# Performance work log

Measured on AMD Instinct MI355X. Metric: run time of the kernel, lower is better.

Reference implementation:

```python
import jax, jax.numpy as jnp
import numpy as np

LN_EPS = 1e-5
K = 6
NUM_KP = 5


def decoder_res_cat(x, w1, b1, gamma, beta, w2, b2):
    # MLP = relu(LayerNorm(Linear(x))); out = Linear(cat([x, MLP(x)]))
    h = x @ w1 + b1
    mu = h.mean(axis=-1, keepdims=True)
    var = ((h - mu) ** 2).mean(axis=-1, keepdims=True)
    h = jax.nn.relu(gamma * (h - mu) / jnp.sqrt(var + LN_EPS) + beta)
    return jnp.concatenate([x, h], axis=-1) @ w2 + b2


def setup_inputs() -> dict:
    key = jax.random.key(0)
    ks = jax.random.split(key, 8)
    B, S, E, H = 2048, 134, 256, 1024
    s = 0.02
    return {
        "hidden_output": jax.random.normal(ks[0], (B, S, E), jnp.float32),
        "future_key_points": jax.random.normal(ks[1], (B, NUM_KP, 2), jnp.float32),
        "ld_w1": jax.random.normal(ks[2], (E, H), jnp.float32) * s,
        "ld_b1": jnp.zeros((H,), jnp.float32),
        "ld_gamma": jnp.ones((H,), jnp.float32),
        "ld_beta": jnp.zeros((H,), jnp.float32),
        "ld_w2": jax.random.normal(ks[3], (E + H, 2 * K), jnp.float32) * s,
        "ld_b2": jnp.zeros((2 * K,), jnp.float32),
        "sd_w1": jax.random.normal(ks[4], (E, H), jnp.float32) * s,
        "sd_b1": jnp.zeros((H,), jnp.float32),
        "sd_gamma": jnp.ones((H,), jnp.float32),
        "sd_beta": jnp.zeros((H,), jnp.float32),
        "sd_w2": jax.random.normal(ks[5], (E + H, K), jnp.float32) * s,
        "sd_b2": jnp.zeros((K,), jnp.float32),
        "context_length": 128,
    }


def reference(hidden_output, future_key_points, ld_w1, ld_b1, ld_gamma, ld_beta,
              ld_w2, ld_b2, sd_w1, sd_b1, sd_gamma, sd_beta, sd_w2, sd_b2,
              context_length):
    B, T = future_key_points.shape[0], future_key_points.shape[1]
    kp_start = context_length - 1  # use_proposal=False
    h = jax.lax.dynamic_slice_in_dim(hidden_output, kp_start, T, axis=1)  # [B,T,E]

    logits = decoder_res_cat(h, ld_w1, ld_b1, ld_gamma, ld_beta, ld_w2, ld_b2)
    logits = logits.reshape(B, T, K, 2)                                   # [B,T,K,2]
    scores = decoder_res_cat(h, sd_w1, sd_b1, sd_gamma, sd_beta, sd_w2, sd_b2)  # [B,T,K]

    # per-mode MSE(reduction='none') summed over xy -> [B,T,K]
    sq = (logits - future_key_points[:, :, None, :2]) ** 2
    loss_bk = sq.sum(axis=-1)
    min_loss = loss_bk.min(axis=-1)           # [B,T]
    min_idx = loss_bk.argmin(axis=-1)         # [B,T] int

    # CrossEntropyLoss applied to softmax(scores) (faithful double-softmax)
    sm = jax.nn.softmax(scores, axis=-1)
    logp = jax.nn.log_softmax(sm, axis=-1)
    ce = -jnp.take_along_axis(logp, min_idx[..., None], axis=-1)[..., 0]  # [B,T]

    weights = 0.1 ** (4.0 - jnp.arange(T, dtype=jnp.float32))             # [T]
    loss_per_kp = min_loss.mean(axis=0) * weights + ce.mean(axis=0)       # [T]

    selected = jnp.take_along_axis(logits, min_idx[:, :, None, None], axis=2)[:, :, 0, :]  # [B,T,2]
    kp_loss = loss_per_kp.mean() * 1.0  # kp_loss_rescale=1.0
    return kp_loss, logits, scores, selected, loss_per_kp
```

## Files before the change

### kernel.cpp

```cpp
#include <hip/hip_runtime.h>
#include <math.h>

#define B_    2048
#define S_    134
#define E_    256
#define H_    1024
#define T_    5
#define KK_   6
#define NROWS (B_*T_)
#define R_    8
#define NBLK  (NROWS/R_)

#define OFF_LOGITS 1
#define OFF_SCORES (OFF_LOGITS + NROWS*12)
#define OFF_SEL    (OFF_SCORES + NROWS*6)
#define OFF_LPK    (OFF_SEL + NROWS*2)

template<int NOUT>
__device__ __forceinline__ void decoder_phase(
    const float (*xs)[E_],
    const float* __restrict__ w1, const float* __restrict__ b1,
    const float* __restrict__ ga, const float* __restrict__ be,
    const float* __restrict__ w2, const float* __restrict__ b2,
    float (*hs)[H_], float (*red)[4][2], float* mu_s, float* rs_s,
    float* osh, float* __restrict__ gout, int g0, int tid)
{
    const int wave = tid >> 6;
    const int lane = tid & 63;
    const int j0   = tid * 4;

    float acc[R_][4];
#pragma unroll
    for (int r = 0; r < R_; ++r) {
        acc[r][0] = 0.f; acc[r][1] = 0.f; acc[r][2] = 0.f; acc[r][3] = 0.f;
    }

    for (int k0 = 0; k0 < E_; k0 += 8) {
        float4 w[8];
#pragma unroll
        for (int kk = 0; kk < 8; ++kk)
            w[kk] = *(const float4*)(w1 + (size_t)(k0 + kk)*H_ + j0);
#pragma unroll
        for (int r = 0; r < R_; ++r) {
            float4 xa = *(const float4*)&xs[r][k0];
            float4 xb = *(const float4*)&xs[r][k0+4];
            acc[r][0] += xa.x*w[0].x; acc[r][1] += xa.x*w[0].y; acc[r][2] += xa.x*w[0].z; acc[r][3] += xa.x*w[0].w;
            acc[r][0] += xa.y*w[1].x; acc[r][1] += xa.y*w[1].y; acc[r][2] += xa.y*w[1].z; acc[r][3] += xa.y*w[1].w;
            acc[r][0] += xa.z*w[2].x; acc[r][1] += xa.z*w[2].y; acc[r][2] += xa.z*w[2].z; acc[r][3] += xa.z*w[2].w;
            acc[r][0] += xa.w*w[3].x; acc[r][1] += xa.w*w[3].y; acc[r][2] += xa.w*w[3].z; acc[r][3] += xa.w*w[3].w;
            acc[r][0] += xb.x*w[4].x; acc[r][1] += xb.x*w[4].y; acc[r][2] += xb.x*w[4].z; acc[r][3] += xb.x*w[4].w;
            acc[r][0] += xb.y*w[5].x; acc[r][1] += xb.y*w[5].y; acc[r][2] += xb.y*w[5].z; acc[r][3] += xb.y*w[5].w;
            acc[r][0] += xb.z*w[6].x; acc[r][1] += xb.z*w[6].y; acc[r][2] += xb.z*w[6].z; acc[r][3] += xb.z*w[6].w;
            acc[r][0] += xb.w*w[7].x; acc[r][1] += xb.w*w[7].y; acc[r][2] += xb.w*w[7].z; acc[r][3] += xb.w*w[7].w;
        }
    }

    {
        float4 bv = *(const float4*)(b1 + j0);
#pragma unroll
        for (int r = 0; r < R_; ++r) {
            acc[r][0] += bv.x; acc[r][1] += bv.y; acc[r][2] += bv.z; acc[r][3] += bv.w;
        }
    }

#pragma unroll
    for (int r = 0; r < R_; ++r) {
        float s  = acc[r][0] + acc[r][1] + acc[r][2] + acc[r][3];
        float ss = acc[r][0]*acc[r][0] + acc[r][1]*acc[r][1]
                 + acc[r][2]*acc[r][2] + acc[r][3]*acc[r][3];
#pragma unroll
        for (int off = 32; off > 0; off >>= 1) {
            s  += __shfl_xor(s,  off, 64);
            ss += __shfl_xor(ss, off, 64);
        }
        if (lane == 0) { red[r][wave][0] = s; red[r][wave][1] = ss; }
    }
    __syncthreads();
    if (tid < R_) {
        float s  = red[tid][0][0] + red[tid][1][0] + red[tid][2][0] + red[tid][3][0];
        float ss = red[tid][0][1] + red[tid][1][1] + red[tid][2][1] + red[tid][3][1];
        float mu  = s * (1.0f / H_);
        float var = ss * (1.0f / H_) - mu * mu;
        mu_s[tid] = mu;
        rs_s[tid] = rsqrtf(var + 1e-5f);
    }
    __syncthreads();

    {
        float4 gv = *(const float4*)(ga + j0);
        float4 bv = *(const float4*)(be + j0);
#pragma unroll
        for (int r = 0; r < R_; ++r) {
            float mu = mu_s[r], rs = rs_s[r];
            float4 hv;
            hv.x = gv.x * ((acc[r][0] - mu) * rs) + bv.x;
            hv.y = gv.y * ((acc[r][1] - mu) * rs) + bv.y;
            hv.z = gv.z * ((acc[r][2] - mu) * rs) + bv.z;
            hv.w = gv.w * ((acc[r][3] - mu) * rs) + bv.w;
            hv.x = hv.x > 0.f ? hv.x : 0.f;
            hv.y = hv.y > 0.f ? hv.y : 0.f;
            hv.z = hv.z > 0.f ? hv.z : 0.f;
            hv.w = hv.w > 0.f ? hv.w : 0.f;
            *(float4*)&hs[r][j0] = hv;
        }
    }
    __syncthreads();

    float p[2][NOUT];
#pragma unroll
    for (int rr = 0; rr < 2; ++rr)
#pragma unroll
        for (int n = 0; n < NOUT; ++n) p[rr][n] = 0.f;

    const int jbase = lane * 20;
#pragma unroll
    for (int jj = 0; jj < 20; ++jj) {
        const int j = jbase + jj;
        float w2r[NOUT];
#pragma unroll
        for (int n = 0; n < NOUT; ++n) w2r[n] = w2[(size_t)j*NOUT + n];
#pragma unroll
        for (int rr = 0; rr < 2; ++rr) {
            const int r = wave*2 + rr;
            float v = (j < E_) ? xs[r][j] : hs[r][j - E_];
#pragma unroll
            for (int n = 0; n < NOUT; ++n) p[rr][n] += v * w2r[n];
        }
    }
#pragma unroll
    for (int rr = 0; rr < 2; ++rr)
#pragma unroll
        for (int n = 0; n < NOUT; ++n)
#pragma unroll
            for (int off = 32; off > 0; off >>= 1)
                p[rr][n] += __shfl_xor(p[rr][n], off, 64);

    if (lane == 0) {
#pragma unroll
        for (int rr = 0; rr < 2; ++rr) {
            const int r = wave*2 + rr;
            const int g = g0 + r;
#pragma unroll
            for (int n = 0; n < NOUT; ++n) {
                float v = p[rr][n] + b2[n];
                osh[r*NOUT + n] = v;
                gout[(size_t)g*NOUT + n] = v;
            }
        }
    }
    __syncthreads();
}

__global__ __launch_bounds__(256, 3)
void kp_fused(const float* __restrict__ hid,  const float* __restrict__ fkp,
              const float* __restrict__ w1ld, const float* __restrict__ b1ld,
              const float* __restrict__ gld,  const float* __restrict__ btld,
              const float* __restrict__ w2ld, const float* __restrict__ b2ld,
              const float* __restrict__ w1sd, const float* __restrict__ b1sd,
              const float* __restrict__ gsd,  const float* __restrict__ btsd,
              const float* __restrict__ w2sd, const float* __restrict__ b2sd,
              const int* __restrict__ ctx,
              float* __restrict__ out, float* __restrict__ ws)
{
    __shared__ float hs[R_][H_];
    __shared__ float xs[R_][E_];
    __shared__ float red[R_][4][2];
    __shared__ float mu_s[R_], rs_s[R_];
    __shared__ float lo_s[R_*12];
    __shared__ float sc_s[R_*6];

    const int tid = threadIdx.x;
    const int g0  = blockIdx.x * R_;
    const int kp0 = ctx[0] - 1;

    {
        const int r   = tid >> 5;
        const int off = (tid & 31) * 8;
        const int g = g0 + r;
        const int b = g / T_;
        const int t = g - b * T_;
        const float* src = hid + (size_t)(b * S_ + kp0 + t) * E_ + off;
        float4 v0 = *(const float4*)(src);
        float4 v1 = *(const float4*)(src + 4);
        *(float4*)&xs[r][off]     = v0;
        *(float4*)&xs[r][off + 4] = v1;
    }
    __syncthreads();

    decoder_phase<12>(xs, w1ld, b1ld, gld, btld, w2ld, b2ld,
                      hs, red, mu_s, rs_s, lo_s, out + OFF_LOGITS, g0, tid);
    decoder_phase<6>(xs, w1sd, b1sd, gsd, btsd, w2sd, b2sd,
                     hs, red, mu_s, rs_s, sc_s, out + OFF_SCORES, g0, tid);

    if (tid < R_) {
        const int g = g0 + tid;
        const int b = g / T_;
        const int t = g - b * T_;
        const float y0 = fkp[b*(T_*2) + t*2 + 0];
        const float y1 = fkp[b*(T_*2) + t*2 + 1];

        float best = 1e30f; int am = 0;
#pragma unroll
        for (int k = 0; k < KK_; ++k) {
            float dx = lo_s[tid*12 + 2*k + 0] - y0;
            float dy = lo_s[tid*12 + 2*k + 1] - y1;
            float L = dx*dx + dy*dy;
            if (L < best) { best = L; am = k; }
        }

        float m = -1e30f;
#pragma unroll
        for (int k = 0; k < KK_; ++k) m = fmaxf(m, sc_s[tid*6 + k]);
        float e[KK_]; float ssum = 0.f;
#pragma unroll
        for (int k = 0; k < KK_; ++k) { e[k] = expf(sc_s[tid*6 + k] - m); ssum += e[k]; }
        const float inv = 1.0f / ssum;
        float lse = 0.f, sm_am = 0.f;
#pragma unroll
        for (int k = 0; k < KK_; ++k) {
            float smk = e[k] * inv;
            lse += expf(smk);
            if (k == am) sm_am = smk;
        }
        const float ce = logf(lse) - sm_am;

        out[OFF_SEL + g*2 + 0] = lo_s[tid*12 + 2*am + 0];
        out[OFF_SEL + g*2 + 1] = lo_s[tid*12 + 2*am + 1];

        atomicAdd(&ws[t],       best);
        atomicAdd(&ws[T_ + t],  ce);
    }
}

__global__ void kp_finalize(const float* __restrict__ ws, float* __restrict__ out)
{
    if (threadIdx.x == 0 && blockIdx.x == 0) {
        const float wts[T_] = {1e-4f, 1e-3f, 1e-2f, 1e-1f, 1.0f};
        float s = 0.f;
#pragma unroll
        for (int t = 0; t < T_; ++t) {
            float ml = ws[t]      * (1.0f / B_);
            float ce = ws[T_ + t] * (1.0f / B_);
            float l  = ml * wts[t] + ce;
            out[OFF_LPK + t] = l;
            s += l;
        }
        out[0] = s * (1.0f / T_);
    }
}

extern "C" void kernel_launch(void* const* d_in, const int* in_sizes, int n_in,
                              void* d_out, int out_size, void* d_ws, size_t ws_size,
                              hipStream_t stream)
{
    const float* hid  = (const float*)d_in[0];
    const float* fkp  = (const float*)d_in[1];
    const float* w1ld = (const float*)d_in[2];
    const float* b1ld = (const float*)d_in[3];
    const float* gld  = (const float*)d_in[4];
    const float* btld = (const float*)d_in[5];
    const float* w2ld = (const float*)d_in[6];
    const float* b2ld = (const float*)d_in[7];
    const float* w1sd = (const float*)d_in[8];
    const float* b1sd = (const float*)d_in[9];
    const float* gsd  = (const float*)d_in[10];
    const float* btsd = (const float*)d_in[11];
    const float* w2sd = (const float*)d_in[12];
    const float* b2sd = (const float*)d_in[13];
    const int*   ctx  = (const int*)d_in[14];
    float* out = (float*)d_out;
    float* ws  = (float*)d_ws;

    hipMemsetAsync(ws, 0, 2 * T_ * sizeof(float), stream);

    kp_fused<<<NBLK, 256, 0, stream>>>(hid, fkp,
                                       w1ld, b1ld, gld, btld, w2ld, b2ld,
                                       w1sd, b1sd, gsd, btsd, w2sd, b2sd,
                                       ctx, out, ws);
    kp_finalize<<<1, 64, 0, stream>>>(ws, out);
}
```

Before: 536.0 us.

## Halve hidden LDS buffer with two-pass second GEMM, double-buffer W1 loads

The hidden activation buffer in shared memory shrinks from 1024 to 512 columns per row. The second linear layer now runs in two passes: the first half of the hidden columns (plus x) is consumed, then the second half is written into the same buffer and consumed. W1 loads in the first GEMM are double-buffered with a software-pipelined prefetch, and launch bounds are raised to 4 blocks per CU. This is meant to cut LDS per block and hide global-load latency so occupancy rises. In exchange it adds extra barriers and may increase register pressure from the second W1 buffer under the tighter occupancy target.

```diff
diff --git a/kernel.cpp b/kernel.cpp
--- a/kernel.cpp
+++ b/kernel.cpp
@@ -5,6 +5,7 @@
 #define S_    134
 #define E_    256
 #define H_    1024
+#define HH_   512
 #define T_    5
 #define KK_   6
 #define NROWS (B_*T_)
@@ -22,7 +23,7 @@
     const float* __restrict__ w1, const float* __restrict__ b1,
     const float* __restrict__ ga, const float* __restrict__ be,
     const float* __restrict__ w2, const float* __restrict__ b2,
-    float (*hs)[H_], float (*red)[4][2], float* mu_s, float* rs_s,
+    float (*hh)[HH_], float (*red)[4][2], float* mu_s, float* rs_s,
     float* osh, float* __restrict__ gout, int g0, int tid)
 {
     const int wave = tid >> 6;
@@ -35,24 +36,38 @@
         acc[r][0] = 0.f; acc[r][1] = 0.f; acc[r][2] = 0.f; acc[r][3] = 0.f;
     }
 
-    for (int k0 = 0; k0 < E_; k0 += 8) {
-        float4 w[8];
+    auto fma8 = [&](const float4 (&W)[8], int koff) {
+#pragma unroll
+        for (int r = 0; r < R_; ++r) {
+            float4 xa = *(const float4*)&xs[r][koff];
+            float4 xb = *(const float4*)&xs[r][koff + 4];
+            acc[r][0] += xa.x*W[0].x; acc[r][1] += xa.x*W[0].y; acc[r][2] += xa.x*W[0].z; acc[r][3] += xa.x*W[0].w;
+            acc[r][0] += xa.y*W[1].x; acc[r][1] += xa.y*W[1].y; acc[r][2] += xa.y*W[1].z; acc[r][3] += xa.y*W[1].w;
+            acc[r][0] += xa.z*W[2].x; acc[r][1] += xa.z*W[2].y; acc[r][2] += xa.z*W[2].z; acc[r][3] += xa.z*W[2].w;
+            acc[r][0] += xa.w*W[3].x; acc[r][1] += xa.w*W[3].y; acc[r][2] += xa.w*W[3].z; acc[r][3] += xa.w*W[3].w;
+            acc[r][0] += xb.x*W[4].x; acc[r][1] += xb.x*W[4].y; acc[r][2] += xb.x*W[4].z; acc[r][3] += xb.x*W[4].w;
+            acc[r][0] += xb.y*W[5].x; acc[r][1] += xb.y*W[5].y; acc[r][2] += xb.y*W[5].z; acc[r][3] += xb.y*W[5].w;
+            acc[r][0] += xb.z*W[6].x; acc[r][1] += xb.z*W[6].y; acc[r][2] += xb.z*W[6].z; acc[r][3] += xb.z*W[6].w;
+            acc[r][0] += xb.w*W[7].x; acc[r][1] += xb.w*W[7].y; acc[r][2] += xb.w*W[7].z; acc[r][3] += xb.w*W[7].w;
+        }
+    };
+
+    float4 wA[8], wB[8];
+#pragma unroll
+    for (int kk = 0; kk < 8; ++kk)
+        wA[kk] = *(const float4*)(w1 + (size_t)kk*H_ + j0);
+
+#pragma unroll 1
+    for (int k0 = 0; k0 < E_; k0 += 16) {
 #pragma unroll
         for (int kk = 0; kk < 8; ++kk)
-            w[kk] = *(const float4*)(w1 + (size_t)(k0 + kk)*H_ + j0);
-#pragma unroll
-        for (int r = 0; r < R_; ++r) {
-            float4 xa = *(const float4*)&xs[r][k0];
-            float4 xb = *(const float4*)&xs[r][k0+4];
-            acc[r][0] += xa.x*w[0].x; acc[r][1] += xa.x*w[0].y; acc[r][2] += xa.x*w[0].z; acc[r][3] += xa.x*w[0].w;
-            acc[r][0] += xa.y*w[1].x; acc[r][1] += xa.y*w[1].y; acc[r][2] += xa.y*w[1].z; acc[r][3] += xa.y*w[1].w;
-            acc[r][0] += xa.z*w[2].x; acc[r][1] += xa.z*w[2].y; acc[r][2] += xa.z*w[2].z; acc[r][3] += xa.z*w[2].w;
-            acc[r][0] += xa.w*w[3].x; acc[r][1] += xa.w*w[3].y; acc[r][2] += xa.w*w[3].z; acc[r][3] += xa.w*w[3].w;
-            acc[r][0] += xb.x*w[4].x; acc[r][1] += xb.x*w[4].y; acc[r][2] += xb.x*w[4].z; acc[r][3] += xb.x*w[4].w;
-            acc[r][0] += xb.y*w[5].x; acc[r][1] += xb.y*w[5].y; acc[r][2] += xb.y*w[5].z; acc[r][3] += xb.y*w[5].w;
-            acc[r][0] += xb.z*w[6].x; acc[r][1] += xb.z*w[6].y; acc[r][2] += xb.z*w[6].z; acc[r][3] += xb.z*w[6].w;
-            acc[r][0] += xb.w*w[7].x; acc[r][1] += xb.w*w[7].y; acc[r][2] += xb.w*w[7].z; acc[r][3] += xb.w*w[7].w;
-        }
+            wB[kk] = *(const float4*)(w1 + (size_t)(k0 + 8 + kk)*H_ + j0);
+        fma8(wA, k0);
+        const int kn = (k0 + 16 < E_) ? (k0 + 16) : 0;
+#pragma unroll
+        for (int kk = 0; kk < 8; ++kk)
+            wA[kk] = *(const float4*)(w1 + (size_t)(kn + kk)*H_ + j0);
+        fma8(wB, k0 + 8);
     }
 
     {
@@ -86,7 +101,7 @@
     }
     __syncthreads();
 
-    {
+    if (j0 < HH_) {
         float4 gv = *(const float4*)(ga + j0);
         float4 bv = *(const float4*)(be + j0);
 #pragma unroll
@@ -101,7 +116,7 @@
             hv.y = hv.y > 0.f ? hv.y : 0.f;
             hv.z = hv.z > 0.f ? hv.z : 0.f;
             hv.w = hv.w > 0.f ? hv.w : 0.f;
-            *(float4*)&hs[r][j0] = hv;
+            *(float4*)&hh[r][j0] = hv;
         }
     }
     __syncthreads();
@@ -112,21 +127,63 @@
 #pragma unroll
         for (int n = 0; n < NOUT; ++n) p[rr][n] = 0.f;
 
-    const int jbase = lane * 20;
-#pragma unroll
-    for (int jj = 0; jj < 20; ++jj) {
-        const int j = jbase + jj;
-        float w2r[NOUT];
-#pragma unroll
-        for (int n = 0; n < NOUT; ++n) w2r[n] = w2[(size_t)j*NOUT + n];
-#pragma unroll
-        for (int rr = 0; rr < 2; ++rr) {
-            const int r = wave*2 + rr;
-            float v = (j < E_) ? xs[r][j] : hs[r][j - E_];
-#pragma unroll
-            for (int n = 0; n < NOUT; ++n) p[rr][n] += v * w2r[n];
-        }
-    }
+    {
+        const int jbase = lane * 12;
+#pragma unroll
+        for (int jj = 0; jj < 12; ++jj) {
+            const int j = jbase + jj;
+            float w2r[NOUT];
+#pragma unroll
+            for (int n = 0; n < NOUT; ++n) w2r[n] = w2[(size_t)j*NOUT + n];
+#pragma unroll
+            for (int rr = 0; rr < 2; ++rr) {
+                const int r = wave*2 + rr;
+                float v = (j < E_) ? xs[r][j] : hh[r][j - E_];
+#pragma unroll
+                for (int n = 0; n < NOUT; ++n) p[rr][n] += v * w2r[n];
+            }
+        }
+    }
+    __syncthreads();
+
+    if (j0 >= HH_) {
+        float4 gv = *(const float4*)(ga + j0);
+        float4 bv = *(const float4*)(be + j0);
+#pragma unroll
+        for (int r = 0; r < R_; ++r) {
+            float mu = mu_s[r], rs = rs_s[r];
+            float4 hv;
+            hv.x = gv.x * ((acc[r][0] - mu) * rs) + bv.x;
+            hv.y = gv.y * ((acc[r][1] - mu) * rs) + bv.y;
+            hv.z = gv.z * ((acc[r][2] - mu) * rs) + bv.z;
+            hv.w = gv.w * ((acc[r][3] - mu) * rs) + bv.w;
+            hv.x = hv.x > 0.f ? hv.x : 0.f;
+            hv.y = hv.y > 0.f ? hv.y : 0.f;
+            hv.z = hv.z > 0.f ? hv.z : 0.f;
+            hv.w = hv.w > 0.f ? hv.w : 0.f;
+            *(float4*)&hh[r][j0 - HH_] = hv;
+        }
+    }
+    __syncthreads();
+
+    {
+        const int jbase = 768 + lane * 8;
+#pragma unroll
+        for (int jj = 0; jj < 8; ++jj) {
+            const int j = jbase + jj;
+            float w2r[NOUT];
+#pragma unroll
+            for (int n = 0; n < NOUT; ++n) w2r[n] = w2[(size_t)j*NOUT + n];
+#pragma unroll
+            for (int rr = 0; rr < 2; ++rr) {
+                const int r = wave*2 + rr;
+                float v = hh[r][j - 768];
+#pragma unroll
+                for (int n = 0; n < NOUT; ++n) p[rr][n] += v * w2r[n];
+            }
+        }
+    }
+
 #pragma unroll
     for (int rr = 0; rr < 2; ++rr)
 #pragma unroll
@@ -151,7 +208,7 @@
     __syncthreads();
 }
 
-__global__ __launch_bounds__(256, 3)
+__global__ __launch_bounds__(256, 4)
 void kp_fused(const float* __restrict__ hid,  const float* __restrict__ fkp,
               const float* __restrict__ w1ld, const float* __restrict__ b1ld,
               const float* __restrict__ gld,  const float* __restrict__ btld,
@@ -162,7 +219,7 @@
               const int* __restrict__ ctx,
               float* __restrict__ out, float* __restrict__ ws)
 {
-    __shared__ float hs[R_][H_];
+    __shared__ float hh[R_][HH_];
     __shared__ float xs[R_][E_];
     __shared__ float red[R_][4][2];
     __shared__ float mu_s[R_], rs_s[R_];
@@ -188,9 +245,9 @@
     __syncthreads();
 
     decoder_phase<12>(xs, w1ld, b1ld, gld, btld, w2ld, b2ld,
-                      hs, red, mu_s, rs_s, lo_s, out + OFF_LOGITS, g0, tid);
+                      hh, red, mu_s, rs_s, lo_s, out + OFF_LOGITS, g0, tid);
     decoder_phase<6>(xs, w1sd, b1sd, gsd, btsd, w2sd, b2sd,
-                     hs, red, mu_s, rs_s, sc_s, out + OFF_SCORES, g0, tid);
+                     hh, red, mu_s, rs_s, sc_s, out + OFF_SCORES, g0, tid);
 
     if (tid < R_) {
         const int g = g0 + tid;
```

Measured after the change: 731.4 us. 36.5% more time.
